# Performance work log

Measured on AMD Instinct MI355X. Metric: run time of the kernel, lower is better.

The kernel has to match this reference:

```python
import jax, jax.numpy as jnp
import numpy as np

B, S, IN, N, OUT = 4, 4096, 1024, 1024, 1024  # state_size == num_heads, head_dim = 1, hippo D = 1


def setup_inputs() -> dict:
    key = jax.random.key(0)
    ks = jax.random.split(key, 6)
    x = jax.random.normal(ks[0], (B, S, IN), dtype=jnp.float32)
    # input_projection: Linear(input_size, state_size, bias=True)
    Wi = jax.random.normal(ks[1], (IN, N), dtype=jnp.float32) / np.sqrt(IN)
    bi = jax.random.normal(ks[2], (N,), dtype=jnp.float32) * 0.01
    # state_weight (N,1,1) -> per-head scalar recurrence weight; hippo_weight (N,1) -> per-head scalar
    w = jax.random.normal(ks[3], (N,), dtype=jnp.float32)
    u = jax.random.normal(ks[4], (N,), dtype=jnp.float32)
    # output_projection: Linear(state_size, output_size, bias=False)
    Wo = jax.random.normal(ks[5], (N, OUT), dtype=jnp.float32) / np.sqrt(N)
    input_state = jnp.zeros((B, N), dtype=jnp.float32)         # (B, N, H=1) squeezed
    hippo_state = jnp.zeros((B, N, 1, 1), dtype=jnp.float32)   # (B, N, H=1, D=1)
    return {"x": x, "Wi": Wi, "bi": bi, "w": w, "u": u, "Wo": Wo,
            "input_state": input_state, "hippo_state": hippo_state}


def reference(x, Wi, bi, w, u, Wo, input_state, hippo_state):
    # input projection then split into N heads of dim 1 -> [B, S, N]
    xp = jnp.einsum("bsi,in->bsn", x, Wi) + bi
    # hippo cross-term: (hippo_state @ hippo_weight) with H=D=1 -> scalar per (b, n).
    # hippo_state is never updated inside the recurrence (torch path), so this is constant over time.
    hippo_term = hippo_state[..., 0, 0] * u  # [B, N]

    def step(h, xt):
        # h_t = tanh(h_{t-1} * w + x_t + hippo_term)   (per-head scalar recurrence, H=1)
        h = jnp.tanh(h * w + xt + hippo_term)
        return h, h

    xs = jnp.swapaxes(xp, 0, 1)  # [S, B, N]
    last_state, ys = jax.lax.scan(step, input_state, xs)
    states = jnp.swapaxes(ys, 0, 1)  # [B, S, N]
    out = jnp.einsum("bsn,no->bso", states, Wo)  # output_projection (no bias)
    output_state = last_state.reshape(B, -1)     # input[:, -1] flattened over (N, H)
    return out, output_state
```

## Files before the change

### kernel.cpp

```cpp
#include <hip/hip_runtime.h>
#include <hip/hip_bf16.h>

using f16x8 = __attribute__((ext_vector_type(8))) _Float16;
using f32x4 = __attribute__((ext_vector_type(4))) float;

extern "C" __device__ float __ocml_native_exp2_f32(float);

static constexpr int Bc = 4, Sc = 4096, INc = 1024, Nc = 1024, OUTc = 1024;
static constexpr int Mc = Bc * Sc;
#define K2LE 2.8853900817779268f

__device__ __forceinline__ unsigned short f2h(float f) {
    return __builtin_bit_cast(unsigned short, (_Float16)f);
}
__device__ __forceinline__ float h2f(unsigned short s) {
    return (float)__builtin_bit_cast(_Float16, s);
}

__global__ __launch_bounds__(256) void split2h(const float* __restrict__ in,
                                               unsigned short* __restrict__ hi,
                                               unsigned short* __restrict__ lo, int n4) {
    int i = blockIdx.x * blockDim.x + threadIdx.x;
    if (i >= n4) return;
    float4 v = reinterpret_cast<const float4*>(in)[i];
    ushort4 h, l;
    h.x = f2h(v.x); l.x = f2h(v.x - h2f(h.x));
    h.y = f2h(v.y); l.y = f2h(v.y - h2f(h.y));
    h.z = f2h(v.z); l.z = f2h(v.z - h2f(h.z));
    h.w = f2h(v.w); l.w = f2h(v.w - h2f(h.w));
    reinterpret_cast<ushort4*>(hi)[i] = h;
    reinterpret_cast<ushort4*>(lo)[i] = l;
}

__global__ __launch_bounds__(256) void tr_h(const float* __restrict__ in,
                                            unsigned short* __restrict__ out, int R, int C) {
    __shared__ float t[32][33];
    int c0 = blockIdx.x * 32, r0 = blockIdx.y * 32;
    for (int i = threadIdx.y; i < 32; i += 8)
        t[i][threadIdx.x] = in[(size_t)(r0 + i) * C + c0 + threadIdx.x];
    __syncthreads();
    for (int i = threadIdx.y; i < 32; i += 8)
        out[(size_t)(c0 + i) * R + r0 + threadIdx.x] = f2h(t[threadIdx.x][i]);
}

template<int MODE>
__global__ __launch_bounds__(256) void gemm_h(const unsigned short* __restrict__ Ah,
                                              const unsigned short* __restrict__ Al,
                                              const unsigned short* __restrict__ BT,
                                              float* __restrict__ C, int N, int K,
                                              const float* __restrict__ bi,
                                              const float* __restrict__ u,
                                              const float* __restrict__ hs,
                                              const float* __restrict__ wv) {
    constexpr int BM = 128, BN = 128, BK = 64;
    __shared__ alignas(16) unsigned short Ash[BM * BK];
    __shared__ alignas(16) unsigned short Asl[MODE ? BM * BK : 1];
    __shared__ alignas(16) unsigned short Bs[BN * BK];
    const int nb = N >> 7;
    const int cpx = (int)gridDim.x >> 3;
    const int wg = (blockIdx.x & 7) * cpx + (blockIdx.x >> 3);
    const int bm = wg / nb, bn = wg % nb;
    const int tid = threadIdx.x;
    const int w = tid >> 6, l = tid & 63;
    const int wr = w >> 1, wc = w & 1;
    const int r = l & 15, g4 = l >> 4;
    const int lrow = l >> 3, lcol = (l & 7) * 8;

    f32x4 acc[4][4] = {};

    const size_t aoff = (size_t)bm * BM * K;
    const size_t boff = (size_t)bn * BN * K;

    for (int k0 = 0; k0 < K; k0 += BK) {
        __syncthreads();
#pragma unroll
        for (int i = 0; i < 4; i++) {
            size_t grow = (size_t)((w * 4 + i) * 8 + lrow) * K + (k0 + lcol);
            int ldst = (w * 4 + i) * 512;
            __builtin_amdgcn_global_load_lds(
                (const __attribute__((address_space(1))) void*)(Ah + aoff + grow),
                (__attribute__((address_space(3))) void*)(Ash + ldst), 16, 0, 0);
            if (MODE)
                __builtin_amdgcn_global_load_lds(
                    (const __attribute__((address_space(1))) void*)(Al + aoff + grow),
                    (__attribute__((address_space(3))) void*)(Asl + ldst), 16, 0, 0);
            __builtin_amdgcn_global_load_lds(
                (const __attribute__((address_space(1))) void*)(BT + boff + grow),
                (__attribute__((address_space(3))) void*)(Bs + ldst), 16, 0, 0);
        }
        __syncthreads();
#pragma unroll
        for (int kk = 0; kk < BK; kk += 32) {
            f16x8 ah[4], al[4], bf[4];
#pragma unroll
            for (int m = 0; m < 4; m++) {
                int off = (wr * 64 + m * 16 + r) * BK + kk + g4 * 8;
                ah[m] = *reinterpret_cast<const f16x8*>(Ash + off);
                if (MODE) al[m] = *reinterpret_cast<const f16x8*>(Asl + off);
            }
#pragma unroll
            for (int n = 0; n < 4; n++)
                bf[n] = *reinterpret_cast<const f16x8*>(Bs + (wc * 64 + n * 16 + r) * BK + kk + g4 * 8);
#pragma unroll
            for (int m = 0; m < 4; m++)
#pragma unroll
                for (int n = 0; n < 4; n++) {
                    acc[m][n] = __builtin_amdgcn_mfma_f32_16x16x32_f16(ah[m], bf[n], acc[m][n], 0, 0, 0);
                    if (MODE)
                        acc[m][n] = __builtin_amdgcn_mfma_f32_16x16x32_f16(al[m], bf[n], acc[m][n], 0, 0, 0);
                }
        }
    }

    const int bbase = MODE ? ((bm * BM) / Sc) * Nc : 0;
#pragma unroll
    for (int m = 0; m < 4; m++) {
        int row = bm * BM + wr * 64 + m * 16 + g4 * 4;
#pragma unroll
        for (int n = 0; n < 4; n++) {
            int col = bn * BN + wc * 64 + n * 16 + r;
            float extra = 0.f;
            if (MODE) extra = bi[col] + hs[bbase + col] * u[col] + wv[col];
#pragma unroll
            for (int q = 0; q < 4; q++) {
                float v = acc[m][n][q];
                if (MODE) v = (v + extra) * K2LE;
                C[(size_t)(row + q) * N + col] = v;
            }
        }
    }
}

static constexpr int SROW = 68;

template<bool PREF>
__device__ __forceinline__ void sblk(const float* __restrict__ xrow,
                                     float (&cur)[32], float (&nxt)[32],
                                     float* __restrict__ hbl, int tblk, float nw2, float& rr) {
#pragma unroll
    for (int d = 0; d < 32; d++) {
        if (PREF) nxt[d] = xrow[(size_t)(tblk + 32 + d) << 10];
        float z = fmaf(nw2, rr, cur[d]);
        float e = __ocml_native_exp2_f32(z);
        rr = __builtin_amdgcn_rcpf(e + 1.f);
        hbl[d * SROW] = rr;
    }
    asm volatile("s_waitcnt lgkmcnt(0)" ::: "memory");
    __builtin_amdgcn_s_barrier();
}

__device__ __forceinline__ unsigned int pk2(float a, float b) {
    return ((unsigned int)f2h(fmaf(-2.f, b, 1.f)) << 16) | f2h(fmaf(-2.f, a, 1.f));
}

__device__ __forceinline__ void drain(const float* __restrict__ buf, int tblk,
                                      unsigned short* __restrict__ srow, int n0, int l) {
    __builtin_amdgcn_s_barrier();
    asm volatile("" ::: "memory");
    int row8 = l >> 3, cg = l & 7;
#pragma unroll
    for (int i = 0; i < 4; i++) {
        int row = i * 8 + row8;
        float4 a = *reinterpret_cast<const float4*>(&buf[row * SROW + cg * 8]);
        float4 b = *reinterpret_cast<const float4*>(&buf[row * SROW + cg * 8 + 4]);
        uint4 v = { pk2(a.x, a.y), pk2(a.z, a.w), pk2(b.x, b.y), pk2(b.z, b.w) };
        *reinterpret_cast<uint4*>(&srow[((size_t)(tblk + row) << 10) + n0 + cg * 8]) = v;
    }
}

__global__ __launch_bounds__(128) void scan4(const float* __restrict__ xp,
                                             const float* __restrict__ w,
                                             const float* __restrict__ h0,
                                             unsigned short* __restrict__ states,
                                             float* __restrict__ out_state) {
    __shared__ alignas(16) float hb[2][32 * SROW];
    const int l = threadIdx.x & 63;
    const int wave = threadIdx.x >> 6;
    const int b = blockIdx.x >> 4;
    const int n0 = (blockIdx.x & 15) * 64;

    if (wave == 0) {
        const int tid = blockIdx.x * 64 + l;
        const int n = tid & (Nc - 1);
        float nw2 = w[n] * (-2.f * K2LE);
        float rr = 0.5f - 0.5f * h0[tid];
        const float* xrow = xp + ((size_t)b << 22) + n;
        float* hbl0 = &hb[0][l];
        float* hbl1 = &hb[1][l];

        float xa[32], xb[32];
#pragma unroll
        for (int d = 0; d < 32; d++) xa[d] = xrow[(size_t)d << 10];

        int t = 0;
        for (; t + 64 < Sc; t += 64) {
            sblk<true>(xrow, xa, xb, hbl0, t, nw2, rr);
            sblk<true>(xrow, xb, xa, hbl1, t + 32, nw2, rr);
        }
        sblk<true >(xrow, xa, xb, hbl0, t, nw2, rr);
        sblk<false>(xrow, xb, xa, hbl1, t + 32, nw2, rr);
        out_state[tid] = fmaf(-2.f, rr, 1.f);
    } else {
        unsigned short* srow = states + ((size_t)b << 22);
        for (int t = 0; t < Sc; t += 64) {
            drain(hb[0], t, srow, n0, l);
            drain(hb[1], t + 32, srow, n0, l);
        }
    }
}

extern "C" void kernel_launch(void* const* d_in, const int* in_sizes, int n_in,
                              void* d_out, int out_size, void* d_ws, size_t ws_size,
                              hipStream_t stream) {
    const float* x  = (const float*)d_in[0];
    const float* Wi = (const float*)d_in[1];
    const float* bi = (const float*)d_in[2];
    const float* w  = (const float*)d_in[3];
    const float* u  = (const float*)d_in[4];
    const float* Wo = (const float*)d_in[5];
    const float* h0 = (const float*)d_in[6];
    const float* hs = (const float*)d_in[7];
    float* out = (float*)d_out;
    float* out_state = out + (size_t)Mc * OUTc;
    float* xp = out;

    char* ws = (char*)d_ws;
    unsigned short* xh  = (unsigned short*)ws;
    unsigned short* xl  = (unsigned short*)(ws + 33554432);
    unsigned short* WiT = (unsigned short*)(ws + 67108864);
    unsigned short* WoT = (unsigned short*)(ws + 69206016);
    unsigned short* states = xh;

    split2h<<<(Mc * INc / 4 + 255) / 256, 256, 0, stream>>>(x, xh, xl, Mc * INc / 4);
    dim3 tb(32, 8);
    tr_h<<<dim3(Nc / 32, INc / 32), tb, 0, stream>>>(Wi, WiT, INc, Nc);
    tr_h<<<dim3(OUTc / 32, Nc / 32), tb, 0, stream>>>(Wo, WoT, Nc, OUTc);

    gemm_h<1><<<(Mc / 128) * (Nc / 128), 256, 0, stream>>>(xh, xl, WiT, xp, Nc, INc, bi, u, hs, w);
    scan4<<<64, 128, 0, stream>>>(xp, w, h0, states, out_state);
    gemm_h<0><<<(Mc / 128) * (OUTc / 128), 256, 0, stream>>>(states, nullptr, WoT, out, OUTc, Nc,
                                                             nullptr, nullptr, nullptr, nullptr);
}
```

Measured before the change: 256.9 us.

## Pack scan waves into fewer large blocks and stage states as fp16 in LDS

The recurrence kernel changes from 64 small blocks (one scan wave plus one drain wave each) to 8 blocks of 1024 threads. Each block holds 8 scan waves and 8 drain waves, each pair with its own LDS double buffer. The scan wave now converts each state to fp16 before writing it to LDS, so the drain waves copy packed halves straight to global memory and LDS traffic is halved. The trade-off is that block-wide barriers now couple all 16 waves, and the whole scan runs on only 8 CUs. The conversion arithmetic also moves onto the serial critical path.

```diff
diff --git a/kernel.cpp b/kernel.cpp
--- a/kernel.cpp
+++ b/kernel.cpp
@@ -131,29 +131,26 @@
     }
 }
 
-static constexpr int SROW = 68;
+static constexpr int SROWS = 72;
 
 template<bool PREF>
 __device__ __forceinline__ void sblk(const float* __restrict__ xrow,
                                      float (&cur)[32], float (&nxt)[32],
-                                     float* __restrict__ hbl, int tblk, float nw2, float& rr) {
+                                     unsigned short* __restrict__ hbl, int tblk,
+                                     float nw2, float& rr) {
 #pragma unroll
     for (int d = 0; d < 32; d++) {
         if (PREF) nxt[d] = xrow[(size_t)(tblk + 32 + d) << 10];
         float z = fmaf(nw2, rr, cur[d]);
         float e = __ocml_native_exp2_f32(z);
         rr = __builtin_amdgcn_rcpf(e + 1.f);
-        hbl[d * SROW] = rr;
+        hbl[d * SROWS] = f2h(fmaf(-2.f, rr, 1.f));
     }
     asm volatile("s_waitcnt lgkmcnt(0)" ::: "memory");
     __builtin_amdgcn_s_barrier();
 }
 
-__device__ __forceinline__ unsigned int pk2(float a, float b) {
-    return ((unsigned int)f2h(fmaf(-2.f, b, 1.f)) << 16) | f2h(fmaf(-2.f, a, 1.f));
-}
-
-__device__ __forceinline__ void drain(const float* __restrict__ buf, int tblk,
+__device__ __forceinline__ void drain(const unsigned short* __restrict__ buf, int tblk,
                                       unsigned short* __restrict__ srow, int n0, int l) {
     __builtin_amdgcn_s_barrier();
     asm volatile("" ::: "memory");
@@ -161,32 +158,31 @@
 #pragma unroll
     for (int i = 0; i < 4; i++) {
         int row = i * 8 + row8;
-        float4 a = *reinterpret_cast<const float4*>(&buf[row * SROW + cg * 8]);
-        float4 b = *reinterpret_cast<const float4*>(&buf[row * SROW + cg * 8 + 4]);
-        uint4 v = { pk2(a.x, a.y), pk2(a.z, a.w), pk2(b.x, b.y), pk2(b.z, b.w) };
+        uint4 v = *reinterpret_cast<const uint4*>(&buf[row * SROWS + cg * 8]);
         *reinterpret_cast<uint4*>(&srow[((size_t)(tblk + row) << 10) + n0 + cg * 8]) = v;
     }
 }
 
-__global__ __launch_bounds__(128) void scan4(const float* __restrict__ xp,
-                                             const float* __restrict__ w,
-                                             const float* __restrict__ h0,
-                                             unsigned short* __restrict__ states,
-                                             float* __restrict__ out_state) {
-    __shared__ alignas(16) float hb[2][32 * SROW];
+__global__ __launch_bounds__(1024) void scan6(const float* __restrict__ xp,
+                                              const float* __restrict__ w,
+                                              const float* __restrict__ h0,
+                                              unsigned short* __restrict__ states,
+                                              float* __restrict__ out_state) {
+    __shared__ alignas(16) unsigned short hb[8][2][32 * SROWS];
     const int l = threadIdx.x & 63;
-    const int wave = threadIdx.x >> 6;
-    const int b = blockIdx.x >> 4;
-    const int n0 = (blockIdx.x & 15) * 64;
-
-    if (wave == 0) {
-        const int tid = blockIdx.x * 64 + l;
-        const int n = tid & (Nc - 1);
+    const int wv = threadIdx.x >> 6;
+    const int p = wv & 7;
+    const int b = blockIdx.x >> 1;
+    const int n0 = (blockIdx.x & 1) * 512 + p * 64;
+
+    if (wv < 8) {
+        const int n = n0 + l;
+        const int tid = (b << 10) + n;
         float nw2 = w[n] * (-2.f * K2LE);
         float rr = 0.5f - 0.5f * h0[tid];
         const float* xrow = xp + ((size_t)b << 22) + n;
-        float* hbl0 = &hb[0][l];
-        float* hbl1 = &hb[1][l];
+        unsigned short* hbl0 = &hb[p][0][l];
+        unsigned short* hbl1 = &hb[p][1][l];
 
         float xa[32], xb[32];
 #pragma unroll
@@ -202,9 +198,11 @@
         out_state[tid] = fmaf(-2.f, rr, 1.f);
     } else {
         unsigned short* srow = states + ((size_t)b << 22);
+        const unsigned short* b0 = hb[p][0];
+        const unsigned short* b1 = hb[p][1];
         for (int t = 0; t < Sc; t += 64) {
-            drain(hb[0], t, srow, n0, l);
-            drain(hb[1], t + 32, srow, n0, l);
+            drain(b0, t, srow, n0, l);
+            drain(b1, t + 32, srow, n0, l);
         }
     }
 }
@@ -237,7 +235,7 @@
     tr_h<<<dim3(OUTc / 32, Nc / 32), tb, 0, stream>>>(Wo, WoT, Nc, OUTc);
 
     gemm_h<1><<<(Mc / 128) * (Nc / 128), 256, 0, stream>>>(xh, xl, WiT, xp, Nc, INc, bi, u, hs, w);
-    scan4<<<64, 128, 0, stream>>>(xp, w, h0, states, out_state);
+    scan6<<<8, 1024, 0, stream>>>(xp, w, h0, states, out_state);
     gemm_h<0><<<(Mc / 128) * (OUTc / 128), 256, 0, stream>>>(states, nullptr, WoT, out, OUTc, Nc,
                                                              nullptr, nullptr, nullptr, nullptr);
 }
```

Measured after the change: 354.0 us. 37.8% more time.
